# Optimization experiments

Measured on AMD Instinct MI355X. Metric: run time of the kernel, lower is better.

## Reference

```python
import jax, jax.numpy as jnp
import numpy as np

B, S, T = 2048, 32, 32
D, H = 128, 256       # cle_dim, rnn_dim
VS, VT = 256, 256     # source/target char vocab
BOW = 1               # MorphoDataset.Factor.BOW


def setup_inputs() -> dict:
    key = jax.random.key(0)
    ks = jax.random.split(key, 16)
    n = lambda k, sh: (jax.random.normal(k, sh, jnp.float32) * 0.05)
    inp = {
        "src_emb": n(ks[0], (VS, D)),
        "tgt_emb": n(ks[1], (VT, D)),
        "enc_f_W": n(ks[2], (D, 3 * H)),
        "enc_f_U": n(ks[3], (H, 3 * H)),
        "enc_f_b": jnp.zeros((2, 3 * H), jnp.float32),
        "enc_b_W": n(ks[4], (D, 3 * H)),
        "enc_b_U": n(ks[5], (H, 3 * H)),
        "enc_b_b": jnp.zeros((2, 3 * H), jnp.float32),
        "dec_W": n(ks[6], (D + H, 3 * H)),
        "dec_U": n(ks[7], (H, 3 * H)),
        "dec_b": jnp.zeros((2, 3 * H), jnp.float32),
        "out_W": n(ks[8], (H, VT)),
        "out_b": jnp.zeros((VT,), jnp.float32),
        "att_src_W": n(ks[9], (H, H)),
        "att_src_b": jnp.zeros((H,), jnp.float32),
        "att_st_W": n(ks[10], (H, H)),
        "att_st_b": jnp.zeros((H,), jnp.float32),
        "att_v": n(ks[11], (H, 1)),
        "att_v_b": jnp.zeros((1,), jnp.float32),
        "source_ids": jax.random.randint(ks[12], (B, S), 0, VS, jnp.int32),
        "target_ids": jax.random.randint(ks[13], (B, T), 0, VT, jnp.int32),
    }
    return inp


def _gru_step(h, x, W, U, b):
    # Keras GRU, reset_after=True: separate input/recurrent biases b[0], b[1]
    gx = x @ W + b[0]
    gh = h @ U + b[1]
    xz, xr, xh = jnp.split(gx, 3, axis=-1)
    hz, hr, hh = jnp.split(gh, 3, axis=-1)
    z = jax.nn.sigmoid(xz + hz)
    r = jax.nn.sigmoid(xr + hr)
    c = jnp.tanh(xh + r * hh)
    return z * h + (1.0 - z) * c


def _gru_scan(x_tbd, W, U, b):
    # x_tbd: [S, B, D] -> outputs [S, B, H]
    h0 = jnp.zeros((x_tbd.shape[1], U.shape[0]), x_tbd.dtype)
    def step(h, x):
        h = _gru_step(h, x, W, U, b)
        return h, h
    _, ys = jax.lax.scan(step, h0, x_tbd)
    return ys


def reference(src_emb, tgt_emb, enc_f_W, enc_f_U, enc_f_b, enc_b_W, enc_b_U, enc_b_b,
              dec_W, dec_U, dec_b, out_W, out_b, att_src_W, att_src_b,
              att_st_W, att_st_b, att_v, att_v_b, source_ids, target_ids):
    # ---- Encoder: bidirectional GRU, merge_mode='sum' ----
    x = src_emb[source_ids]                      # [B, S, D]
    x_t = jnp.transpose(x, (1, 0, 2))            # [S, B, D]
    fwd = _gru_scan(x_t, enc_f_W, enc_f_U, enc_f_b)
    bwd = _gru_scan(x_t[::-1], enc_b_W, enc_b_U, enc_b_b)[::-1]
    source_states = jnp.transpose(fwd + bwd, (1, 0, 2))  # [B, S, H]

    # projected source states are constant across decoder steps -> precompute
    proj_src = source_states @ att_src_W + att_src_b     # [B, S, H]

    def attend(inp, h):
        p = h @ att_st_W + att_st_b                      # [B, H]
        e = jnp.tanh(proj_src + p[:, None, :]) @ att_v + att_v_b  # [B, S, 1]
        w = jax.nn.softmax(e, axis=1)                    # softmax over source positions
        ctx = jnp.sum(source_states * w, axis=1)         # [B, H]
        return jnp.concatenate([inp, ctx], axis=1)       # [B, D+H]

    # ---- Decoder (teacher forcing) ----
    h0 = source_states[:, 0]                             # [B, H]
    bow = jnp.broadcast_to(tgt_emb[BOW], (source_ids.shape[0], tgt_emb.shape[1]))
    inp0 = attend(bow, h0)

    def dstep(carry, tgt_t):
        h, inp = carry
        h = _gru_step(h, inp, dec_W, dec_U, dec_b)       # GRUCell step
        logits = h @ out_W + out_b                       # [B, VT]
        nxt = attend(tgt_emb[tgt_t], h)
        return (h, nxt), logits

    _, logits = jax.lax.scan(dstep, (h0, inp0), jnp.transpose(target_ids))
    return jnp.transpose(logits, (1, 0, 2))              # [B, T, VT]
```

## Files before the change

### kernel.cpp

```cpp
#include <hip/hip_runtime.h>
#include <math.h>

#define B_  2048
#define S_  32
#define T_  32
#define D_  128
#define H_  256
#define G3  768
#define VT_ 256

typedef __attribute__((ext_vector_type(8))) short short8;
typedef __attribute__((ext_vector_type(4))) float f32x4;
typedef __attribute__((ext_vector_type(4))) unsigned short us4;
typedef __attribute__((ext_vector_type(8))) unsigned short us8;

__device__ inline unsigned short f2bf(float x) {
  union { float f; unsigned u; } v; v.f = x;
  unsigned r = v.u + 0x7FFFu + ((v.u >> 16) & 1u);
  return (unsigned short)(r >> 16);
}
__device__ inline float bf2f(unsigned short b) {
  union { unsigned u; float f; } v; v.u = ((unsigned)b) << 16;
  return v.f;
}

struct Leg {
  const float* A;
  const float* Bw;
  const float* bias;
  float*       C;
  const int*   rowIdx;
  int idxStride;
  int N, K, lda, ldb, ldc;
};

#define BM 128
#define BN 128
#define BK 32

__device__ inline int swz(int row) { return ((row ^ (row >> 3)) & 7) << 3; }

__global__ __launch_bounds__(256)
void gemm_legs(Leg l0, Leg l1, Leg l2, Leg l3) {
  Leg L = (blockIdx.z == 0) ? l0 : (blockIdx.z == 1) ? l1 : (blockIdx.z == 2) ? l2 : l3;
  int n0 = blockIdx.x * BN;
  if (n0 >= L.N) return;
  int m0 = blockIdx.y * BM;

  __shared__ unsigned short As[BM * 64];
  __shared__ unsigned short Bs[BN * 64];

  int tid = threadIdx.x;
  int a_row = tid >> 3;
  int a_k4  = (tid & 7) * 4;
  int b_n = tid & 127;
  int b_h = tid >> 7;

  int lane = tid & 63;
  int wv = tid >> 6;
  int wr = (wv >> 1) * 64;
  int wc = (wv & 1) * 64;
  int fr = lane & 15;
  int fk = (lane >> 4) * 8;

  f32x4 acc[4][4];
  #pragma unroll
  for (int m = 0; m < 4; m++)
    #pragma unroll
    for (int n = 0; n < 4; n++)
      acc[m][n] = (f32x4){0.f, 0.f, 0.f, 0.f};

  size_t a_base[4];
  #pragma unroll
  for (int i = 0; i < 4; i++) {
    int m = m0 + a_row + 32 * i;
    int ar = L.rowIdx ? L.rowIdx[(size_t)m * L.idxStride] : m;
    a_base[i] = (size_t)ar * L.lda;
  }

  for (int k0 = 0; k0 < L.K; k0 += BK) {
    f32x4 av[4];
    #pragma unroll
    for (int i = 0; i < 4; i++)
      av[i] = *(const f32x4*)(L.A + a_base[i] + k0 + a_k4);
    float bv[16];
    #pragma unroll
    for (int kk = 0; kk < 16; kk++)
      bv[kk] = L.Bw[(size_t)(k0 + b_h * 16 + kk) * L.ldb + n0 + b_n];

    if (k0) __syncthreads();

    #pragma unroll
    for (int i = 0; i < 4; i++) {
      int r = a_row + 32 * i;
      int sw = swz(r);
      us4 hv, lv;
      #pragma unroll
      for (int j = 0; j < 4; j++) {
        float x = av[i][j];
        unsigned short h = f2bf(x);
        hv[j] = h;
        lv[j] = f2bf(x - bf2f(h));
      }
      *(us4*)&As[(r * 64 + a_k4) ^ sw]      = hv;
      *(us4*)&As[(r * 64 + 32 + a_k4) ^ sw] = lv;
    }
    {
      int r = b_n;
      int sw = swz(r);
      us8 h0, h1, l0v, l1v;
      #pragma unroll
      for (int kk = 0; kk < 8; kk++) {
        unsigned short h = f2bf(bv[kk]);
        h0[kk] = h; l0v[kk] = f2bf(bv[kk] - bf2f(h));
        unsigned short h2 = f2bf(bv[kk + 8]);
        h1[kk] = h2; l1v[kk] = f2bf(bv[kk + 8] - bf2f(h2));
      }
      int kbase = b_h * 16;
      *(us8*)&Bs[(r * 64 + kbase) ^ sw]          = h0;
      *(us8*)&Bs[(r * 64 + kbase + 8) ^ sw]      = h1;
      *(us8*)&Bs[(r * 64 + 32 + kbase) ^ sw]     = l0v;
      *(us8*)&Bs[(r * 64 + 32 + kbase + 8) ^ sw] = l1v;
    }
    __syncthreads();

    short8 bhi[4], blo[4];
    #pragma unroll
    for (int n = 0; n < 4; n++) {
      int r = wc + n * 16 + fr;
      int sw = swz(r);
      bhi[n] = *(const short8*)&Bs[(r * 64 + fk) ^ sw];
      blo[n] = *(const short8*)&Bs[(r * 64 + 32 + fk) ^ sw];
    }
    #pragma unroll
    for (int m = 0; m < 4; m++) {
      int r = wr + m * 16 + fr;
      int sw = swz(r);
      short8 ahi = *(const short8*)&As[(r * 64 + fk) ^ sw];
      short8 alo = *(const short8*)&As[(r * 64 + 32 + fk) ^ sw];
      #pragma unroll
      for (int n = 0; n < 4; n++) {
        acc[m][n] = __builtin_amdgcn_mfma_f32_16x16x32_bf16(ahi, bhi[n], acc[m][n], 0, 0, 0);
        acc[m][n] = __builtin_amdgcn_mfma_f32_16x16x32_bf16(ahi, blo[n], acc[m][n], 0, 0, 0);
        acc[m][n] = __builtin_amdgcn_mfma_f32_16x16x32_bf16(alo, bhi[n], acc[m][n], 0, 0, 0);
      }
    }
  }

  int rbase = (lane >> 4) * 4;
  #pragma unroll
  for (int m = 0; m < 4; m++) {
    #pragma unroll
    for (int rr = 0; rr < 4; rr++) {
      int row = m0 + wr + m * 16 + rbase + rr;
      #pragma unroll
      for (int n = 0; n < 4; n++) {
        int col = n0 + wc + n * 16 + fr;
        float v = acc[m][n][rr];
        if (L.bias) v += L.bias[col];
        L.C[(size_t)row * L.ldc + col] = v;
      }
    }
  }
}

__device__ inline float sigm(float x) { return 1.f / (1.f + expf(-x)); }

__global__ __launch_bounds__(256)
void enc_gate(const float* __restrict__ gxf, const float* __restrict__ ghf,
              const float* __restrict__ gxb, const float* __restrict__ ghb,
              float* __restrict__ hf, float* __restrict__ hb,
              float* __restrict__ ss, int s) {
  int idx = blockIdx.x * 256 + threadIdx.x;
  int dir = blockIdx.y;
  const float* gx = dir ? gxb : gxf;
  const float* gh = dir ? ghb : ghf;
  float* h = dir ? hb : hf;
  int b = idx >> 8, j = idx & 255;
  size_t g = (size_t)b * G3 + j;
  float z = sigm(gx[g] + gh[g]);
  float r = sigm(gx[g + H_] + gh[g + H_]);
  float c = tanhf(gx[g + 2 * H_] + r * gh[g + 2 * H_]);
  float hn = z * h[idx] + (1.f - z) * c;
  h[idx] = hn;
  int pos = dir ? (S_ - 1 - s) : s;
  ss[((size_t)pos * B_ + b) * H_ + j] += hn;
}

__global__ __launch_bounds__(256)
void dec_gate(const float* __restrict__ gx, const float* __restrict__ gc,
              const float* __restrict__ gh,
              const float* __restrict__ h_in, float* __restrict__ h_out) {
  int idx = blockIdx.x * 256 + threadIdx.x;
  int b = idx >> 8, j = idx & 255;
  size_t g = (size_t)b * G3 + j;
  float xz = gx[g] + gc[g];
  float xr = gx[g + H_] + gc[g + H_];
  float xh = gx[g + 2 * H_] + gc[g + 2 * H_];
  float z = sigm(xz + gh[g]);
  float r = sigm(xr + gh[g + H_]);
  float c = tanhf(xh + r * gh[g + 2 * H_]);
  h_out[idx] = z * h_in[idx] + (1.f - z) * c;
}

__global__ __launch_bounds__(256)
void attend_k(const float* __restrict__ proj, const float* __restrict__ ss,
              const float* __restrict__ p, const float* __restrict__ att_v,
              float* __restrict__ ctx) {
  int b = blockIdx.x;
  int tid = threadIdx.x;
  int lane = tid & 63;
  int wv = tid >> 6;
  __shared__ float e_s[S_];
  __shared__ float w_s[S_];
  float pq[4], vq[4];
  #pragma unroll
  for (int q = 0; q < 4; q++) {
    pq[q] = p[(size_t)b * H_ + q * 64 + lane];
    vq[q] = att_v[q * 64 + lane];
  }
  #pragma unroll
  for (int i = 0; i < 8; i++) {
    int s = wv * 8 + i;
    const float* pr = proj + ((size_t)s * B_ + b) * H_;
    float part = 0.f;
    #pragma unroll
    for (int q = 0; q < 4; q++)
      part += tanhf(pr[q * 64 + lane] + pq[q]) * vq[q];
    #pragma unroll
    for (int off = 32; off; off >>= 1)
      part += __shfl_xor(part, off);
    if (lane == 0) e_s[s] = part;
  }
  __syncthreads();
  float m = -1e30f;
  #pragma unroll
  for (int s = 0; s < S_; s++) m = fmaxf(m, e_s[s]);
  float den = 0.f;
  #pragma unroll
  for (int s = 0; s < S_; s++) den += expf(e_s[s] - m);
  if (tid < S_) w_s[tid] = expf(e_s[tid] - m) / den;
  __syncthreads();
  float acc = 0.f;
  #pragma unroll
  for (int s = 0; s < S_; s++)
    acc = fmaf(w_s[s], ss[((size_t)s * B_ + b) * H_ + tid], acc);
  ctx[(size_t)b * H_ + tid] = acc;
}

extern "C" void kernel_launch(void* const* d_in, const int* in_sizes, int n_in,
                              void* d_out, int out_size, void* d_ws, size_t ws_size,
                              hipStream_t stream) {
  const float* src_emb   = (const float*)d_in[0];
  const float* tgt_emb   = (const float*)d_in[1];
  const float* enc_f_W   = (const float*)d_in[2];
  const float* enc_f_U   = (const float*)d_in[3];
  const float* enc_f_b   = (const float*)d_in[4];
  const float* enc_b_W   = (const float*)d_in[5];
  const float* enc_b_U   = (const float*)d_in[6];
  const float* enc_b_b   = (const float*)d_in[7];
  const float* dec_W     = (const float*)d_in[8];
  const float* dec_U     = (const float*)d_in[9];
  const float* dec_b     = (const float*)d_in[10];
  const float* out_W     = (const float*)d_in[11];
  const float* out_b     = (const float*)d_in[12];
  const float* att_src_W = (const float*)d_in[13];
  const float* att_src_b = (const float*)d_in[14];
  const float* att_st_W  = (const float*)d_in[15];
  const float* att_st_b  = (const float*)d_in[16];
  const float* att_v     = (const float*)d_in[17];
  const int* source_ids  = (const int*)d_in[19];
  const int* target_ids  = (const int*)d_in[20];
  float* out = (float*)d_out;

  float* w = (float*)d_ws;
  size_t off = 0;
  auto alloc = [&](size_t n) { float* p = w + off; off += n; return p; };
  float* ss   = alloc((size_t)S_ * B_ * H_);
  float* proj = alloc((size_t)S_ * B_ * H_);
  float* hf   = alloc((size_t)B_ * H_);
  float* hb   = alloc((size_t)B_ * H_);
  float* g0   = alloc((size_t)B_ * G3);
  float* g1   = alloc((size_t)B_ * G3);
  float* g2   = alloc((size_t)B_ * G3);
  float* g3   = alloc((size_t)B_ * G3);
  float* hdec = alloc((size_t)B_ * H_);
  float* ctx  = alloc((size_t)B_ * H_);
  float* pbuf = alloc((size_t)B_ * H_);

  hipMemsetAsync(ss, 0, (size_t)S_ * B_ * H_ * sizeof(float), stream);
  hipMemsetAsync(hf, 0, (size_t)B_ * H_ * sizeof(float), stream);
  hipMemsetAsync(hb, 0, (size_t)B_ * H_ * sizeof(float), stream);

  Leg Z = {};

  for (int s = 0; s < S_; s++) {
    Leg gxf = { src_emb, enc_f_W, enc_f_b,      g0, source_ids + s,            S_, G3, D_, D_, G3, G3 };
    Leg ghf = { hf,      enc_f_U, enc_f_b + G3, g1, nullptr,                   0,  G3, H_, H_, G3, G3 };
    Leg gxb = { src_emb, enc_b_W, enc_b_b,      g2, source_ids + (S_ - 1 - s), S_, G3, D_, D_, G3, G3 };
    Leg ghb = { hb,      enc_b_U, enc_b_b + G3, g3, nullptr,                   0,  G3, H_, H_, G3, G3 };
    gemm_legs<<<dim3(G3 / BN, B_ / BM, 4), 256, 0, stream>>>(gxf, ghf, gxb, ghb);
    enc_gate<<<dim3((B_ * H_) / 256, 2), 256, 0, stream>>>(g0, g1, g2, g3, hf, hb, ss, s);
  }

  {
    Leg pr = { ss, att_src_W, att_src_b, proj, nullptr, 0, H_, H_, H_, H_, H_ };
    gemm_legs<<<dim3(H_ / BN, (S_ * B_) / BM, 1), 256, 0, stream>>>(pr, Z, Z, Z);
  }

  {
    Leg p0 = { ss, att_st_W, att_st_b, pbuf, nullptr, 0, H_, H_, H_, H_, H_ };
    gemm_legs<<<dim3(H_ / BN, B_ / BM, 1), 256, 0, stream>>>(p0, Z, Z, Z);
    attend_k<<<B_, 256, 0, stream>>>(proj, ss, pbuf, att_v, ctx);
  }

  for (int t = 0; t < T_; t++) {
    const float* hprev = (t == 0) ? ss : hdec;
    Leg GH = { hprev, dec_U, dec_b + G3, g1, nullptr, 0, G3, H_, H_, G3, G3 };
    Leg GC = { ctx, dec_W + (size_t)D_ * G3, nullptr, g2, nullptr, 0, G3, H_, H_, G3, G3 };
    Leg GX;
    if (t == 0) {
      GX = { tgt_emb + 1 * D_ , dec_W, dec_b, g0, nullptr, 0, G3, D_, 0, G3, G3 };
    } else {
      GX = { tgt_emb, dec_W, dec_b, g0, target_ids + (t - 1), T_, G3, D_, D_, G3, G3 };
    }
    gemm_legs<<<dim3(G3 / BN, B_ / BM, 3), 256, 0, stream>>>(GH, GC, GX, Z);
    dec_gate<<<(B_ * H_) / 256, 256, 0, stream>>>(g0, g2, g1, hprev, hdec);

    Leg LO = { hdec, out_W, out_b, out + (size_t)t * VT_, nullptr, 0, VT_, H_, H_, VT_, T_ * VT_ };
    Leg LP = { hdec, att_st_W, att_st_b, pbuf, nullptr, 0, H_, H_, H_, H_, H_ };
    gemm_legs<<<dim3(VT_ / BN, B_ / BM, 2), 256, 0, stream>>>(LO, LP, Z, Z);

    if (t < T_ - 1)
      attend_k<<<B_, 256, 0, stream>>>(proj, ss, pbuf, att_v, ctx);
  }
}
```

Measured before the change: 3.866 ms.

## Fuse GRU gate GEMMs with gate math and pre-split weights into bf16 planes

Replaces the per-step separate GEMM + gate kernels with a single gru_step kernel that computes all three gate blocks for a tile and applies the GRU nonlinearity in the epilogue. Weights and embeddings are transposed and split into bf16 hi/lo planes once up front, and hidden states are written directly as hi/lo planes, so the per-tile fp32-to-bf16 conversion disappears. Projected source states are stored in bf16 and the two attention projections share one launch. The intent is to cut kernel launches and intermediate gate buffer traffic, at the cost of lower precision in proj (single bf16) and a smaller 64x64 tile per block.

```diff
diff --git a/kernel.cpp b/kernel.cpp
--- a/kernel.cpp
+++ b/kernel.cpp
@@ -8,134 +8,137 @@
 #define H_  256
 #define G3  768
 #define VT_ 256
+#define BOW_ 1
 
 typedef __attribute__((ext_vector_type(8))) short short8;
 typedef __attribute__((ext_vector_type(4))) float f32x4;
 typedef __attribute__((ext_vector_type(4))) unsigned short us4;
 typedef __attribute__((ext_vector_type(8))) unsigned short us8;
-
-__device__ inline unsigned short f2bf(float x) {
+typedef unsigned short u16;
+
+__device__ inline u16 f2bf(float x) {
   union { float f; unsigned u; } v; v.f = x;
   unsigned r = v.u + 0x7FFFu + ((v.u >> 16) & 1u);
-  return (unsigned short)(r >> 16);
-}
-__device__ inline float bf2f(unsigned short b) {
-  union { unsigned u; float f; } v; v.u = ((unsigned)b) << 16;
-  return v.f;
-}
-
-struct Leg {
-  const float* A;
-  const float* Bw;
-  const float* bias;
-  float*       C;
-  const int*   rowIdx;
-  int idxStride;
-  int N, K, lda, ldb, ldc;
+  return (u16)(r >> 16);
+}
+__device__ inline float bf2f(u16 b) {
+  union { unsigned u; float f; } v; v.u = ((unsigned)b) << 16; return v.f;
+}
+__device__ inline int swz(int r) { return ((r ^ (r >> 3)) & 7) << 3; }
+__device__ inline float sigm(float x) { return 1.f / (1.f + expf(-x)); }
+
+struct TMat { const float* src; u16* dhi; u16* dlo; int R; int C; int tile0; };
+struct TPack { TMat m[10]; };
+
+__global__ __launch_bounds__(256)
+void wsplit_t(TPack P) {
+  int bx = blockIdx.x;
+  TMat M = P.m[0];
+  #pragma unroll
+  for (int i = 1; i < 10; i++) if (bx >= P.m[i].tile0) M = P.m[i];
+  int ti = bx - M.tile0;
+  int tilesR = M.R >> 6;
+  int rt = ti % tilesR, ct = ti / tilesR;
+  int r0 = rt * 64, c0 = ct * 64;
+  __shared__ float ts[64][65];
+  int tid = threadIdx.x;
+  int cx = tid & 63, ry = tid >> 6;
+  #pragma unroll
+  for (int i = 0; i < 16; i++) {
+    int r = ry * 16 + i;
+    ts[r][cx] = M.src[(size_t)(r0 + r) * M.C + c0 + cx];
+  }
+  __syncthreads();
+  int rx = tid & 63, cy = tid >> 6;
+  #pragma unroll
+  for (int i = 0; i < 16; i++) {
+    int cc = cy * 16 + i;
+    float v = ts[rx][cc];
+    u16 hi = f2bf(v);
+    size_t o = (size_t)(c0 + cc) * M.R + r0 + rx;
+    M.dhi[o] = hi;
+    M.dlo[o] = f2bf(v - bf2f(hi));
+  }
+}
+
+__global__ __launch_bounds__(256)
+void esplit(const float* a, const float* b, u16* ah, u16* al, u16* bh, u16* bl, int n) {
+  int i = blockIdx.x * 256 + threadIdx.x;
+  if (i >= 2 * n) return;
+  const float* s = (i < n) ? a : b;
+  u16* dh = (i < n) ? ah : bh;
+  u16* dl = (i < n) ? al : bl;
+  int j = (i < n) ? i : i - n;
+  float v = s[j];
+  u16 hi = f2bf(v);
+  dh[j] = hi; dl[j] = f2bf(v - bf2f(hi));
+}
+
+struct PLeg {
+  const u16* Ahi; const u16* Alo; const float* Af32; int lda;
+  const u16* Bthi; const u16* Btlo; int ldb;
+  const float* bias; void* C; int ldc; int cmode;
+  int M, N, K;
 };
 
-#define BM 128
-#define BN 128
-#define BK 32
-
-__device__ inline int swz(int row) { return ((row ^ (row >> 3)) & 7) << 3; }
-
 __global__ __launch_bounds__(256)
-void gemm_legs(Leg l0, Leg l1, Leg l2, Leg l3) {
-  Leg L = (blockIdx.z == 0) ? l0 : (blockIdx.z == 1) ? l1 : (blockIdx.z == 2) ? l2 : l3;
-  int n0 = blockIdx.x * BN;
-  if (n0 >= L.N) return;
-  int m0 = blockIdx.y * BM;
-
-  __shared__ unsigned short As[BM * 64];
-  __shared__ unsigned short Bs[BN * 64];
-
+void gemm_pl(PLeg l0, PLeg l1) {
+  PLeg L = blockIdx.z ? l1 : l0;
+  int n0 = blockIdx.x * 128; if (n0 >= L.N) return;
+  int m0 = blockIdx.y * 128; if (m0 >= L.M) return;
+  __shared__ u16 As[128 * 64];
+  __shared__ u16 Bs[128 * 64];
   int tid = threadIdx.x;
-  int a_row = tid >> 3;
-  int a_k4  = (tid & 7) * 4;
-  int b_n = tid & 127;
-  int b_h = tid >> 7;
-
-  int lane = tid & 63;
-  int wv = tid >> 6;
-  int wr = (wv >> 1) * 64;
-  int wc = (wv & 1) * 64;
-  int fr = lane & 15;
-  int fk = (lane >> 4) * 8;
-
+  int lane = tid & 63, wv = tid >> 6;
+  int wr = (wv >> 1) * 64, wc = (wv & 1) * 64;
+  int fr = lane & 15, fk = (lane >> 4) * 8;
   f32x4 acc[4][4];
   #pragma unroll
   for (int m = 0; m < 4; m++)
     #pragma unroll
-    for (int n = 0; n < 4; n++)
-      acc[m][n] = (f32x4){0.f, 0.f, 0.f, 0.f};
-
-  size_t a_base[4];
-  #pragma unroll
-  for (int i = 0; i < 4; i++) {
-    int m = m0 + a_row + 32 * i;
-    int ar = L.rowIdx ? L.rowIdx[(size_t)m * L.idxStride] : m;
-    a_base[i] = (size_t)ar * L.lda;
-  }
-
-  for (int k0 = 0; k0 < L.K; k0 += BK) {
-    f32x4 av[4];
-    #pragma unroll
-    for (int i = 0; i < 4; i++)
-      av[i] = *(const f32x4*)(L.A + a_base[i] + k0 + a_k4);
-    float bv[16];
-    #pragma unroll
-    for (int kk = 0; kk < 16; kk++)
-      bv[kk] = L.Bw[(size_t)(k0 + b_h * 16 + kk) * L.ldb + n0 + b_n];
-
+    for (int n = 0; n < 4; n++) acc[m][n] = (f32x4){0.f, 0.f, 0.f, 0.f};
+
+  int s_row = tid >> 1, s_part = tid & 1;
+
+  for (int k0 = 0; k0 < L.K; k0 += 32) {
     if (k0) __syncthreads();
-
-    #pragma unroll
-    for (int i = 0; i < 4; i++) {
-      int r = a_row + 32 * i;
-      int sw = swz(r);
-      us4 hv, lv;
-      #pragma unroll
-      for (int j = 0; j < 4; j++) {
-        float x = av[i][j];
-        unsigned short h = f2bf(x);
-        hv[j] = h;
-        lv[j] = f2bf(x - bf2f(h));
+    int swA = swz(s_row);
+    if (L.Af32) {
+      const float* src = L.Af32 + (size_t)(m0 + s_row) * L.lda + k0 + s_part * 16;
+      #pragma unroll
+      for (int q = 0; q < 4; q++) {
+        f32x4 v = *(const f32x4*)(src + q * 4);
+        us4 hv, lv;
+        #pragma unroll
+        for (int j = 0; j < 4; j++) {
+          u16 h = f2bf(v[j]); hv[j] = h; lv[j] = f2bf(v[j] - bf2f(h));
+        }
+        *(us4*)&As[(s_row * 64 + s_part * 16 + q * 4) ^ swA]      = hv;
+        *(us4*)&As[(s_row * 64 + 32 + s_part * 16 + q * 4) ^ swA] = lv;
       }
-      *(us4*)&As[(r * 64 + a_k4) ^ sw]      = hv;
-      *(us4*)&As[(r * 64 + 32 + a_k4) ^ sw] = lv;
+    } else {
+      const u16* src = (s_part ? L.Alo : L.Ahi) + (size_t)(m0 + s_row) * L.lda + k0;
+      #pragma unroll
+      for (int q = 0; q < 4; q++)
+        *(us8*)&As[(s_row * 64 + s_part * 32 + q * 8) ^ swA] = *(const us8*)(src + q * 8);
     }
     {
-      int r = b_n;
-      int sw = swz(r);
-      us8 h0, h1, l0v, l1v;
-      #pragma unroll
-      for (int kk = 0; kk < 8; kk++) {
-        unsigned short h = f2bf(bv[kk]);
-        h0[kk] = h; l0v[kk] = f2bf(bv[kk] - bf2f(h));
-        unsigned short h2 = f2bf(bv[kk + 8]);
-        h1[kk] = h2; l1v[kk] = f2bf(bv[kk + 8] - bf2f(h2));
-      }
-      int kbase = b_h * 16;
-      *(us8*)&Bs[(r * 64 + kbase) ^ sw]          = h0;
-      *(us8*)&Bs[(r * 64 + kbase + 8) ^ sw]      = h1;
-      *(us8*)&Bs[(r * 64 + 32 + kbase) ^ sw]     = l0v;
-      *(us8*)&Bs[(r * 64 + 32 + kbase + 8) ^ sw] = l1v;
+      const u16* src = (s_part ? L.Btlo : L.Bthi) + (size_t)(n0 + s_row) * L.ldb + k0;
+      #pragma unroll
+      for (int q = 0; q < 4; q++)
+        *(us8*)&Bs[(s_row * 64 + s_part * 32 + q * 8) ^ swA] = *(const us8*)(src + q * 8);
     }
     __syncthreads();
-
     short8 bhi[4], blo[4];
     #pragma unroll
     for (int n = 0; n < 4; n++) {
-      int r = wc + n * 16 + fr;
-      int sw = swz(r);
-      bhi[n] = *(const short8*)&Bs[(r * 64 + fk) ^ sw];
-      blo[n] = *(const short8*)&Bs[(r * 64 + 32 + fk) ^ sw];
+      int c = wc + n * 16 + fr; int sw = swz(c);
+      bhi[n] = *(const short8*)&Bs[(c * 64 + fk) ^ sw];
+      blo[n] = *(const short8*)&Bs[(c * 64 + 32 + fk) ^ sw];
     }
     #pragma unroll
     for (int m = 0; m < 4; m++) {
-      int r = wr + m * 16 + fr;
-      int sw = swz(r);
+      int r = wr + m * 16 + fr; int sw = swz(r);
       short8 ahi = *(const short8*)&As[(r * 64 + fk) ^ sw];
       short8 alo = *(const short8*)&As[(r * 64 + 32 + fk) ^ sw];
       #pragma unroll
@@ -146,10 +149,9 @@
       }
     }
   }
-
   int rbase = (lane >> 4) * 4;
   #pragma unroll
-  for (int m = 0; m < 4; m++) {
+  for (int m = 0; m < 4; m++)
     #pragma unroll
     for (int rr = 0; rr < 4; rr++) {
       int row = m0 + wr + m * 16 + rbase + rr;
@@ -158,55 +160,144 @@
         int col = n0 + wc + n * 16 + fr;
         float v = acc[m][n][rr];
         if (L.bias) v += L.bias[col];
-        L.C[(size_t)row * L.ldc + col] = v;
+        if (L.cmode == 0) ((float*)L.C)[(size_t)row * L.ldc + col] = v;
+        else              ((u16*)L.C)[(size_t)row * L.ldc + col] = f2bf(v);
       }
     }
-  }
-}
-
-__device__ inline float sigm(float x) { return 1.f / (1.f + expf(-x)); }
+}
+
+struct Seg {
+  const u16* Ahi; const u16* Alo; int lda;
+  const u16* Bthi; const u16* Btlo; int ldb;
+  int K; int gmode;
+};
+struct StepDesc {
+  Seg seg[3]; int nseg;
+  const float* b0; const float* b1;
+  const float* hold; float* hnew;
+  u16* hh; u16* hl;
+  float* ssf; int ssmode;
+  u16* ss0h; u16* ss0l; int writeSS0;
+  const int* ids; int sidx;
+};
 
 __global__ __launch_bounds__(256)
-void enc_gate(const float* __restrict__ gxf, const float* __restrict__ ghf,
-              const float* __restrict__ gxb, const float* __restrict__ ghb,
-              float* __restrict__ hf, float* __restrict__ hb,
-              float* __restrict__ ss, int s) {
-  int idx = blockIdx.x * 256 + threadIdx.x;
-  int dir = blockIdx.y;
-  const float* gx = dir ? gxb : gxf;
-  const float* gh = dir ? ghb : ghf;
-  float* h = dir ? hb : hf;
-  int b = idx >> 8, j = idx & 255;
-  size_t g = (size_t)b * G3 + j;
-  float z = sigm(gx[g] + gh[g]);
-  float r = sigm(gx[g + H_] + gh[g + H_]);
-  float c = tanhf(gx[g + 2 * H_] + r * gh[g + 2 * H_]);
-  float hn = z * h[idx] + (1.f - z) * c;
-  h[idx] = hn;
-  int pos = dir ? (S_ - 1 - s) : s;
-  ss[((size_t)pos * B_ + b) * H_ + j] += hn;
+void gru_step(StepDesc d0, StepDesc d1) {
+  StepDesc D = blockIdx.z ? d1 : d0;
+  int j0 = blockIdx.x * 64;
+  int m0 = blockIdx.y * 64;
+  __shared__ u16 As[64 * 64];
+  __shared__ u16 Bs[3 * 64 * 64];
+  int tid = threadIdx.x;
+  int lane = tid & 63, wv = tid >> 6;
+  int wr = (wv >> 1) * 32, wc = (wv & 1) * 32;
+  int fr = lane & 15, fk = (lane >> 4) * 8;
+  f32x4 acc[4][2][2];
+  #pragma unroll
+  for (int a = 0; a < 4; a++)
+    #pragma unroll
+    for (int m = 0; m < 2; m++)
+      #pragma unroll
+      for (int n = 0; n < 2; n++) acc[a][m][n] = (f32x4){0.f, 0.f, 0.f, 0.f};
+
+  int a_row = tid >> 2, a_part = (tid >> 1) & 1, a_half = tid & 1;
+
+  #pragma unroll
+  for (int sg = 0; sg < 3; sg++) {
+    if (sg < D.nseg) {
+      Seg S = D.seg[sg];
+      int grow = m0 + a_row;
+      int arow;
+      if (S.gmode == 0)      arow = grow;
+      else if (S.gmode == 1) arow = D.ids[grow * S_ + D.sidx];
+      else if (S.gmode == 2) arow = D.ids[grow * S_ + (S_ - 1 - D.sidx)];
+      else                   arow = (D.sidx == 0) ? BOW_ : D.ids[grow * T_ + D.sidx - 1];
+      const u16* Ap = a_part ? S.Alo : S.Ahi;
+      for (int k0 = 0; k0 < S.K; k0 += 32) {
+        if (!(sg == 0 && k0 == 0)) __syncthreads();
+        {
+          int sw = swz(a_row);
+          const u16* src = Ap + (size_t)arow * S.lda + k0 + a_half * 16;
+          int bse = a_row * 64 + a_part * 32 + a_half * 16;
+          *(us8*)&As[(bse + 0) ^ sw] = *(const us8*)(src);
+          *(us8*)&As[(bse + 8) ^ sw] = *(const us8*)(src + 8);
+        }
+        #pragma unroll
+        for (int st = 0; st < 3; st++) {
+          int n768 = st * H_ + j0 + a_row;
+          const u16* srcB = (a_part ? S.Btlo : S.Bthi) + (size_t)n768 * S.ldb + k0 + a_half * 16;
+          int sw = swz(a_row);
+          int bse = a_row * 64 + a_part * 32 + a_half * 16;
+          *(us8*)&Bs[st * 4096 + ((bse + 0) ^ sw)] = *(const us8*)(srcB);
+          *(us8*)&Bs[st * 4096 + ((bse + 8) ^ sw)] = *(const us8*)(srcB + 8);
+        }
+        __syncthreads();
+        short8 ah[2], al[2];
+        #pragma unroll
+        for (int m = 0; m < 2; m++) {
+          int r = wr + m * 16 + fr; int sw = swz(r);
+          ah[m] = *(const short8*)&As[(r * 64 + fk) ^ sw];
+          al[m] = *(const short8*)&As[(r * 64 + 32 + fk) ^ sw];
+        }
+        #pragma unroll
+        for (int st = 0; st < 3; st++) {
+          int ai = (st < 2) ? st : (sg == 0 ? 2 : 3);
+          #pragma unroll
+          for (int n = 0; n < 2; n++) {
+            int c = wc + n * 16 + fr; int sw = swz(c);
+            short8 bh = *(const short8*)&Bs[st * 4096 + ((c * 64 + fk) ^ sw)];
+            short8 bl = *(const short8*)&Bs[st * 4096 + ((c * 64 + 32 + fk) ^ sw)];
+            #pragma unroll
+            for (int m = 0; m < 2; m++) {
+              acc[ai][m][n] = __builtin_amdgcn_mfma_f32_16x16x32_bf16(ah[m], bh, acc[ai][m][n], 0, 0, 0);
+              acc[ai][m][n] = __builtin_amdgcn_mfma_f32_16x16x32_bf16(ah[m], bl, acc[ai][m][n], 0, 0, 0);
+              acc[ai][m][n] = __builtin_amdgcn_mfma_f32_16x16x32_bf16(al[m], bh, acc[ai][m][n], 0, 0, 0);
+            }
+          }
+        }
+      }
+    }
+  }
+
+  int rbase = (lane >> 4) * 4;
+  #pragma unroll
+  for (int m = 0; m < 2; m++)
+    #pragma unroll
+    for (int rr = 0; rr < 4; rr++) {
+      int b = m0 + wr + m * 16 + rbase + rr;
+      #pragma unroll
+      for (int n = 0; n < 2; n++) {
+        int j = j0 + wc + n * 16 + fr;
+        float az  = acc[0][m][n][rr];
+        float ar  = acc[1][m][n][rr];
+        float ahc = acc[2][m][n][rr];
+        float axc = acc[3][m][n][rr];
+        float z = sigm(az + D.b0[j] + D.b1[j]);
+        float r = sigm(ar + D.b0[H_ + j] + D.b1[H_ + j]);
+        float c = tanhf(axc + D.b0[2 * H_ + j] + r * (ahc + D.b1[2 * H_ + j]));
+        size_t o = (size_t)b * H_ + j;
+        float hn = z * D.hold[o] + (1.f - z) * c;
+        D.hnew[o] = hn;
+        u16 hi = f2bf(hn);
+        D.hh[o] = hi; D.hl[o] = f2bf(hn - bf2f(hi));
+        if (D.ssmode == 1) {
+          D.ssf[o] = hn;
+        } else if (D.ssmode == 2) {
+          float v = D.ssf[o] + hn;
+          D.ssf[o] = v;
+          if (D.writeSS0) {
+            u16 vh = f2bf(v);
+            D.ss0h[o] = vh; D.ss0l[o] = f2bf(v - bf2f(vh));
+          }
+        }
+      }
+    }
 }
 
 __global__ __launch_bounds__(256)
-void dec_gate(const float* __restrict__ gx, const float* __restrict__ gc,
-              const float* __restrict__ gh,
-              const float* __restrict__ h_in, float* __restrict__ h_out) {
-  int idx = blockIdx.x * 256 + threadIdx.x;
-  int b = idx >> 8, j = idx & 255;
-  size_t g = (size_t)b * G3 + j;
-  float xz = gx[g] + gc[g];
-  float xr = gx[g + H_] + gc[g + H_];
-  float xh = gx[g + 2 * H_] + gc[g + 2 * H_];
-  float z = sigm(xz + gh[g]);
-  float r = sigm(xr + gh[g + H_]);
-  float c = tanhf(xh + r * gh[g + 2 * H_]);
-  h_out[idx] = z * h_in[idx] + (1.f - z) * c;
-}
-
-__global__ __launch_bounds__(256)
-void attend_k(const float* __restrict__ proj, const float* __restrict__ ss,
+void attend_k(const u16* __restrict__ projbf, const float* __restrict__ ss,
               const float* __restrict__ p, const float* __restrict__ att_v,
-              float* __restrict__ ctx) {
+              u16* __restrict__ ctxh, u16* __restrict__ ctxl) {
   int b = blockIdx.x;
   int tid = threadIdx.x;
   int lane = tid & 63;
@@ -222,11 +313,11 @@
   #pragma unroll
   for (int i = 0; i < 8; i++) {
     int s = wv * 8 + i;
-    const float* pr = proj + ((size_t)s * B_ + b) * H_;
+    const u16* pr = projbf + ((size_t)s * B_ + b) * H_;
     float part = 0.f;
     #pragma unroll
     for (int q = 0; q < 4; q++)
-      part += tanhf(pr[q * 64 + lane] + pq[q]) * vq[q];
+      part += tanhf(bf2f(pr[q * 64 + lane]) + pq[q]) * vq[q];
     #pragma unroll
     for (int off = 32; off; off >>= 1)
       part += __shfl_xor(part, off);
@@ -245,7 +336,9 @@
   #pragma unroll
   for (int s = 0; s < S_; s++)
     acc = fmaf(w_s[s], ss[((size_t)s * B_ + b) * H_ + tid], acc);
-  ctx[(size_t)b * H_ + tid] = acc;
+  u16 hi = f2bf(acc);
+  size_t o = (size_t)b * H_ + tid;
+  ctxh[o] = hi; ctxl[o] = f2bf(acc - bf2f(hi));
 }
 
 extern "C" void kernel_launch(void* const* d_in, const int* in_sizes, int n_in,
@@ -273,65 +366,119 @@
   const int* target_ids  = (const int*)d_in[20];
   float* out = (float*)d_out;
 
-  float* w = (float*)d_ws;
+  char* base = (char*)d_ws;
   size_t off = 0;
-  auto alloc = [&](size_t n) { float* p = w + off; off += n; return p; };
-  float* ss   = alloc((size_t)S_ * B_ * H_);
-  float* proj = alloc((size_t)S_ * B_ * H_);
-  float* hf   = alloc((size_t)B_ * H_);
-  float* hb   = alloc((size_t)B_ * H_);
-  float* g0   = alloc((size_t)B_ * G3);
-  float* g1   = alloc((size_t)B_ * G3);
-  float* g2   = alloc((size_t)B_ * G3);
-  float* g3   = alloc((size_t)B_ * G3);
-  float* hdec = alloc((size_t)B_ * H_);
-  float* ctx  = alloc((size_t)B_ * H_);
-  float* pbuf = alloc((size_t)B_ * H_);
-
-  hipMemsetAsync(ss, 0, (size_t)S_ * B_ * H_ * sizeof(float), stream);
-  hipMemsetAsync(hf, 0, (size_t)B_ * H_ * sizeof(float), stream);
-  hipMemsetAsync(hb, 0, (size_t)B_ * H_ * sizeof(float), stream);
-
-  Leg Z = {};
+  auto allocB = [&](size_t bytes) { void* p = base + off; off = (off + bytes + 255) & ~255UL; return p; };
+  const size_t BH = (size_t)B_ * H_;
+
+  float* ss    = (float*)allocB((size_t)S_ * BH * 4);
+  u16*  projbf = (u16*) allocB((size_t)S_ * BH * 2);
+  float* pbuf  = (float*)allocB(BH * 4);
+  u16* ctxh = (u16*)allocB(BH * 2);
+  u16* ctxl = (u16*)allocB(BH * 2);
+  u16* ss0h = (u16*)allocB(BH * 2);
+  u16* ss0l = (u16*)allocB(BH * 2);
+  float* hEncF[2][2]; u16* hEncH[2][2]; u16* hEncL[2][2];
+  for (int d = 0; d < 2; d++)
+    for (int p = 0; p < 2; p++) {
+      hEncF[d][p] = (float*)allocB(BH * 4);
+      hEncH[d][p] = (u16*)allocB(BH * 2);
+      hEncL[d][p] = (u16*)allocB(BH * 2);
+    }
+  float* hDecF[2]; u16* hDecH[2]; u16* hDecL[2];
+  for (int p = 0; p < 2; p++) {
+    hDecF[p] = (float*)allocB(BH * 4);
+    hDecH[p] = (u16*)allocB(BH * 2);
+    hDecL[p] = (u16*)allocB(BH * 2);
+  }
+  auto planes2 = [&](size_t n, u16*& h, u16*& l) { h = (u16*)allocB(n * 2); l = (u16*)allocB(n * 2); };
+  u16 *UtFh,*UtFl,*UtBh,*UtBl,*WtFh,*WtFl,*WtBh,*WtBl;
+  u16 *dUth,*dUtl,*dWcth,*dWctl,*dWxth,*dWxtl;
+  u16 *oWth,*oWtl,*aStth,*aSttl,*aSrth,*aSrtl;
+  u16 *sEh,*sEl,*tEh,*tEl;
+  planes2((size_t)G3*H_, UtFh, UtFl);   planes2((size_t)G3*H_, UtBh, UtBl);
+  planes2((size_t)G3*D_, WtFh, WtFl);   planes2((size_t)G3*D_, WtBh, WtBl);
+  planes2((size_t)G3*H_, dUth, dUtl);   planes2((size_t)G3*H_, dWcth, dWctl);
+  planes2((size_t)G3*D_, dWxth, dWxtl);
+  planes2((size_t)H_*VT_, oWth, oWtl);
+  planes2((size_t)H_*H_, aStth, aSttl); planes2((size_t)H_*H_, aSrth, aSrtl);
+  planes2((size_t)VT_*D_, sEh, sEl);    planes2((size_t)VT_*D_, tEh, tEl);
+
+  TPack P;
+  P.m[0] = { enc_f_U,            UtFh, UtFl, 256, 768, 0   };
+  P.m[1] = { enc_b_U,            UtBh, UtBl, 256, 768, 48  };
+  P.m[2] = { dec_U,              dUth, dUtl, 256, 768, 96  };
+  P.m[3] = { dec_W + 128 * G3,   dWcth, dWctl, 256, 768, 144 };
+  P.m[4] = { enc_f_W,            WtFh, WtFl, 128, 768, 192 };
+  P.m[5] = { enc_b_W,            WtBh, WtBl, 128, 768, 216 };
+  P.m[6] = { dec_W,              dWxth, dWxtl, 128, 768, 240 };
+  P.m[7] = { out_W,              oWth, oWtl, 256, 256, 264 };
+  P.m[8] = { att_st_W,           aStth, aSttl, 256, 256, 280 };
+  P.m[9] = { att_src_W,          aSrth, aSrtl, 256, 256, 296 };
+  wsplit_t<<<312, 256, 0, stream>>>(P);
+  esplit<<<(2 * VT_ * D_ + 255) / 256, 256, 0, stream>>>(src_emb, tgt_emb, sEh, sEl, tEh, tEl, VT_ * D_);
+
+  for (int d = 0; d < 2; d++) {
+    hipMemsetAsync(hEncF[d][0], 0, BH * 4, stream);
+    hipMemsetAsync(hEncH[d][0], 0, BH * 2, stream);
+    hipMemsetAsync(hEncL[d][0], 0, BH * 2, stream);
+  }
 
   for (int s = 0; s < S_; s++) {
-    Leg gxf = { src_emb, enc_f_W, enc_f_b,      g0, source_ids + s,            S_, G3, D_, D_, G3, G3 };
-    Leg ghf = { hf,      enc_f_U, enc_f_b + G3, g1, nullptr,                   0,  G3, H_, H_, G3, G3 };
-    Leg gxb = { src_emb, enc_b_W, enc_b_b,      g2, source_ids + (S_ - 1 - s), S_, G3, D_, D_, G3, G3 };
-    Leg ghb = { hb,      enc_b_U, enc_b_b + G3, g3, nullptr,                   0,  G3, H_, H_, G3, G3 };
-    gemm_legs<<<dim3(G3 / BN, B_ / BM, 4), 256, 0, stream>>>(gxf, ghf, gxb, ghb);
-    enc_gate<<<dim3((B_ * H_) / 256, 2), 256, 0, stream>>>(g0, g1, g2, g3, hf, hb, ss, s);
+    int p = s & 1;
+    StepDesc dd[2];
+    for (int d = 0; d < 2; d++) {
+      StepDesc& D = dd[d];
+      D.seg[0] = { hEncH[d][p], hEncL[d][p], H_, d ? UtBh : UtFh, d ? UtBl : UtFl, H_, H_, 0 };
+      D.seg[1] = { sEh, sEl, D_, d ? WtBh : WtFh, d ? WtBl : WtFl, D_, D_, d ? 2 : 1 };
+      D.seg[2] = D.seg[1];
+      D.nseg = 2;
+      D.b0 = d ? enc_b_b : enc_f_b;
+      D.b1 = (d ? enc_b_b : enc_f_b) + G3;
+      D.hold = hEncF[d][p]; D.hnew = hEncF[d][p ^ 1];
+      D.hh = hEncH[d][p ^ 1]; D.hl = hEncL[d][p ^ 1];
+      int pos = d ? (S_ - 1 - s) : s;
+      D.ssf = ss + (size_t)pos * BH;
+      D.ssmode = (s < S_ / 2) ? 1 : 2;
+      D.ss0h = ss0h; D.ss0l = ss0l;
+      D.writeSS0 = (d == 1 && s == S_ - 1) ? 1 : 0;
+      D.ids = source_ids; D.sidx = s;
+    }
+    gru_step<<<dim3(4, 32, 2), 256, 0, stream>>>(dd[0], dd[1]);
   }
 
   {
-    Leg pr = { ss, att_src_W, att_src_b, proj, nullptr, 0, H_, H_, H_, H_, H_ };
-    gemm_legs<<<dim3(H_ / BN, (S_ * B_) / BM, 1), 256, 0, stream>>>(pr, Z, Z, Z);
-  }
-
-  {
-    Leg p0 = { ss, att_st_W, att_st_b, pbuf, nullptr, 0, H_, H_, H_, H_, H_ };
-    gemm_legs<<<dim3(H_ / BN, B_ / BM, 1), 256, 0, stream>>>(p0, Z, Z, Z);
-    attend_k<<<B_, 256, 0, stream>>>(proj, ss, pbuf, att_v, ctx);
-  }
+    PLeg proj = { nullptr, nullptr, ss, H_, aSrth, aSrtl, H_, att_src_b,
+                  projbf, H_, 1, S_ * B_, H_, H_ };
+    PLeg p0   = { nullptr, nullptr, ss, H_, aStth, aSttl, H_, att_st_b,
+                  pbuf, H_, 0, B_, H_, H_ };
+    gemm_pl<<<dim3(2, 512, 2), 256, 0, stream>>>(proj, p0);
+  }
+  attend_k<<<B_, 256, 0, stream>>>(projbf, ss, pbuf, att_v, ctxh, ctxl);
 
   for (int t = 0; t < T_; t++) {
-    const float* hprev = (t == 0) ? ss : hdec;
-    Leg GH = { hprev, dec_U, dec_b + G3, g1, nullptr, 0, G3, H_, H_, G3, G3 };
-    Leg GC = { ctx, dec_W + (size_t)D_ * G3, nullptr, g2, nullptr, 0, G3, H_, H_, G3, G3 };
-    Leg GX;
-    if (t == 0) {
-      GX = { tgt_emb + 1 * D_ , dec_W, dec_b, g0, nullptr, 0, G3, D_, 0, G3, G3 };
-    } else {
-      GX = { tgt_emb, dec_W, dec_b, g0, target_ids + (t - 1), T_, G3, D_, D_, G3, G3 };
-    }
-    gemm_legs<<<dim3(G3 / BN, B_ / BM, 3), 256, 0, stream>>>(GH, GC, GX, Z);
-    dec_gate<<<(B_ * H_) / 256, 256, 0, stream>>>(g0, g2, g1, hprev, hdec);
-
-    Leg LO = { hdec, out_W, out_b, out + (size_t)t * VT_, nullptr, 0, VT_, H_, H_, VT_, T_ * VT_ };
-    Leg LP = { hdec, att_st_W, att_st_b, pbuf, nullptr, 0, H_, H_, H_, H_, H_ };
-    gemm_legs<<<dim3(VT_ / BN, B_ / BM, 2), 256, 0, stream>>>(LO, LP, Z, Z);
+    int p = t & 1;
+    StepDesc D;
+    D.seg[0] = { t ? hDecH[p] : ss0h, t ? hDecL[p] : ss0l, H_, dUth, dUtl, H_, H_, 0 };
+    D.seg[1] = { ctxh, ctxl, H_, dWcth, dWctl, H_, H_, 0 };
+    D.seg[2] = { tEh, tEl, D_, dWxth, dWxtl, D_, D_, 3 };
+    D.nseg = 3;
+    D.b0 = dec_b; D.b1 = dec_b + G3;
+    D.hold = t ? hDecF[p] : ss;
+    D.hnew = hDecF[p ^ 1];
+    D.hh = hDecH[p ^ 1]; D.hl = hDecL[p ^ 1];
+    D.ssf = nullptr; D.ssmode = 0;
+    D.ss0h = nullptr; D.ss0l = nullptr; D.writeSS0 = 0;
+    D.ids = target_ids; D.sidx = t;
+    gru_step<<<dim3(4, 32, 1), 256, 0, stream>>>(D, D);
+
+    PLeg LO = { hDecH[p ^ 1], hDecL[p ^ 1], nullptr, H_, oWth, oWtl, H_, out_b,
+                out + (size_t)t * VT_, T_ * VT_, 0, B_, VT_, H_ };
+    PLeg LP = { hDecH[p ^ 1], hDecL[p ^ 1], nullptr, H_, aStth, aSttl, H_, att_st_b,
+                pbuf, H_, 0, B_, H_, H_ };
+    gemm_pl<<<dim3(2, 16, 2), 256, 0, stream>>>(LO, LP);
 
     if (t < T_ - 1)
-      attend_k<<<B_, 256, 0, stream>>>(proj, ss, pbuf, att_v, ctx);
-  }
-}
+      attend_k<<<B_, 256, 0, stream>>>(projbf, ss, pbuf, att_v, ctxh, ctxl);
+  }
+}
```

Result: slower. 4.048 ms (+4.7%).
